# Performance work log

Hardware: AMD Instinct MI355X
Metric: run time of the kernel (lower is better)

## Reference

```python
import jax, jax.numpy as jnp
import numpy as np

H = 1024
N_HEADS = 8
HEAD_DIM = H // N_HEADS
META_DIM = 256
VOCAB = 32000
MIN_W, MAX_W = 0.1, 5.0
LN_EPS = 1e-5


def _ln(x, g, b):
    mu = jnp.mean(x, axis=-1, keepdims=True)
    var = jnp.var(x, axis=-1, keepdims=True)
    return (x - mu) * jax.lax.rsqrt(var + LN_EPS) * g + b


def setup_inputs() -> dict:
    key = jax.random.key(0)
    ks = jax.random.split(key, 16)
    B, S = 4, 2048
    s = 0.02
    return {
        "hidden_states": jax.random.normal(ks[0], (B, S, H), jnp.float32),
        "token_ids": jax.random.randint(ks[1], (B, S), 0, VOCAB, jnp.int32),
        "attention_mask": jnp.ones((B, S), jnp.bool_),
        "pos_embed": jax.random.normal(ks[2], (1, S, H), jnp.float32),
        # torch nn.MultiheadAttention params
        "in_proj_w": jax.random.normal(ks[3], (3 * H, H), jnp.float32) * s,
        "in_proj_b": jnp.zeros((3 * H,), jnp.float32),
        "out_w": jax.random.normal(ks[4], (H, H), jnp.float32) * s,
        "out_b": jnp.zeros((H,), jnp.float32),
        # meta_network params (torch Linear convention: y = x @ W.T + b)
        "w1": jax.random.normal(ks[5], (META_DIM, 2 * H), jnp.float32) * s,
        "b1": jnp.zeros((META_DIM,), jnp.float32),
        "g1": jnp.ones((META_DIM,), jnp.float32),
        "beta1": jnp.zeros((META_DIM,), jnp.float32),
        "w2": jax.random.normal(ks[6], (META_DIM // 2, META_DIM), jnp.float32) * s,
        "b2": jnp.zeros((META_DIM // 2,), jnp.float32),
        "g2": jnp.ones((META_DIM // 2,), jnp.float32),
        "beta2": jnp.zeros((META_DIM // 2,), jnp.float32),
        "w3": jax.random.normal(ks[7], (1, META_DIM // 2), jnp.float32) * s,
        "b3": jnp.zeros((1,), jnp.float32),
        # tensorized ImportanceMemory.get_importance: one scalar per vocab id
        "importance_table": jax.random.uniform(ks[8], (VOCAB,), jnp.float32) * 0.1,
    }


def reference(hidden_states, token_ids, attention_mask, pos_embed,
              in_proj_w, in_proj_b, out_w, out_b,
              w1, b1, g1, beta1, w2, b2, g2, beta2, w3, b3,
              importance_table):
    B, S, _ = hidden_states.shape
    x = hidden_states + pos_embed[:, :S, :]

    # MultiheadAttention (batch_first, eval mode -> no dropout)
    qkv = x @ in_proj_w.T + in_proj_b                      # [B,S,3H]
    q, k, v = jnp.split(qkv, 3, axis=-1)
    q = q.reshape(B, S, N_HEADS, HEAD_DIM)
    k = k.reshape(B, S, N_HEADS, HEAD_DIM)
    v = v.reshape(B, S, N_HEADS, HEAD_DIM)
    scores = jnp.einsum('bqhd,bkhd->bhqk', q, k) / jnp.sqrt(jnp.float32(HEAD_DIM))
    scores = jnp.where(attention_mask[:, None, None, :], scores, jnp.float32(-1e9))
    attn = jax.nn.softmax(scores, axis=-1)
    ctx = jnp.einsum('bhqk,bkhd->bqhd', attn, v).reshape(B, S, H)
    attended = ctx @ out_w.T + out_b

    combined = jnp.concatenate([x, attended], axis=-1)     # [B,S,2H]
    h = jax.nn.relu(_ln(combined @ w1.T + b1, g1, beta1))
    h = jax.nn.relu(_ln(h @ w2.T + b2, g2, beta2))
    base_weights = (h @ w3.T + b3).squeeze(-1)             # [B,S]

    # tensorized per-token importance lookup + clamp (manual_weights empty)
    importance = importance_table[token_ids]               # gather [B,S]
    weight = jnp.clip(base_weights * (1.0 + importance), MIN_W, MAX_W)
    return jnp.where(attention_mask, weight, 0.0)
```

## Files before the change

### kernel.cpp

```cpp
#include <hip/hip_runtime.h>
#include <hip/hip_bf16.h>
#include <math.h>

typedef __bf16 bf16;
typedef bf16 bf16x8 __attribute__((ext_vector_type(8)));
typedef bf16 bf16x4 __attribute__((ext_vector_type(4)));
typedef float f32x4 __attribute__((ext_vector_type(4)));

#define HDIM 1024
#define NHEADS 8
#define HD 128
#define MD1 256
#define MD2 128
#define LNEPS 1e-5f

__device__ __forceinline__ f32x4 mfma16(bf16x8 a, bf16x8 b, f32x4 c) {
  return __builtin_amdgcn_mfma_f32_16x16x32_bf16(a, b, c, 0, 0, 0);
}

__device__ __forceinline__ void gload_lds16(const bf16* g, bf16* l) {
  __builtin_amdgcn_global_load_lds(
      (const __attribute__((address_space(1))) void*)g,
      (__attribute__((address_space(3))) void*)l, 16, 0, 0);
}

__global__ __launch_bounds__(256) void k_prep_all(
    const float* __restrict__ hs, const float* __restrict__ pos,
    bf16* __restrict__ xbf, int SH, int nprep,
    const float* __restrict__ inwf, bf16* __restrict__ winp, int n0,
    const float* __restrict__ w1f, bf16* __restrict__ w1b, int n2,
    const float* __restrict__ w2f, bf16* __restrict__ w2b, int n3,
    const float* __restrict__ owf, const float* __restrict__ obf,
    const float* __restrict__ b1f, bf16* __restrict__ Wp,
    float* __restrict__ b1p, int blocks_el) {
  const int bid = blockIdx.x;
  const int tid = threadIdx.x;
  if (bid < blocks_el) {
    int i = (bid * 256 + tid) * 4;
    if (i < nprep) {
      float4 a = *(const float4*)(hs + i);
      float4 p = *(const float4*)(pos + (i % SH));
      bf16x4 o;
      o[0] = (bf16)(a.x + p.x); o[1] = (bf16)(a.y + p.y);
      o[2] = (bf16)(a.z + p.z); o[3] = (bf16)(a.w + p.w);
      *(bf16x4*)(xbf + i) = o;
      return;
    }
    int j = i - nprep;
    const float* s; bf16* d;
    if (j < n0)           { s = inwf + j; d = winp + j; }
    else if (j < n0 + n2) { s = w1f + (j - n0); d = w1b + (j - n0); }
    else                  { s = w2f + (j - n0 - n2); d = w2b + (j - n0 - n2); }
    float4 v = *(const float4*)s;
    bf16x4 o;
    o[0] = (bf16)v.x; o[1] = (bf16)v.y; o[2] = (bf16)v.z; o[3] = (bf16)v.w;
    *(bf16x4*)d = o;
    return;
  }
  if (bid < blocks_el + 64) {
    __shared__ bf16 Bst[64][42];
    const int bid2 = bid - blocks_el;
    const int d0 = (bid2 & 15) * 64, n0w = (bid2 >> 4) * 64;
    const int w = tid >> 6, lane = tid & 63;
    const int quad = lane >> 4, l16 = lane & 15;
    const float* arow = w1f + (size_t)(n0w + w * 16 + l16) * 2048 + 1024;
    f32x4 acc[4] = {};
    for (int k0 = 0; k0 < 1024; k0 += 32) {
      const int kk = tid >> 3, dd8 = (tid & 7) * 8;
      float4 va = *(const float4*)(owf + (size_t)(k0 + kk) * 1024 + d0 + dd8);
      float4 vb = *(const float4*)(owf + (size_t)(k0 + kk) * 1024 + d0 + dd8 + 4);
      __syncthreads();
      Bst[dd8 + 0][kk] = (bf16)va.x; Bst[dd8 + 1][kk] = (bf16)va.y;
      Bst[dd8 + 2][kk] = (bf16)va.z; Bst[dd8 + 3][kk] = (bf16)va.w;
      Bst[dd8 + 4][kk] = (bf16)vb.x; Bst[dd8 + 5][kk] = (bf16)vb.y;
      Bst[dd8 + 6][kk] = (bf16)vb.z; Bst[dd8 + 7][kk] = (bf16)vb.w;
      __syncthreads();
      float4 fa = *(const float4*)(arow + k0 + quad * 8);
      float4 fb = *(const float4*)(arow + k0 + quad * 8 + 4);
      bf16x8 af;
      af[0] = (bf16)fa.x; af[1] = (bf16)fa.y; af[2] = (bf16)fa.z; af[3] = (bf16)fa.w;
      af[4] = (bf16)fb.x; af[5] = (bf16)fb.y; af[6] = (bf16)fb.z; af[7] = (bf16)fb.w;
#pragma unroll
      for (int dg = 0; dg < 4; ++dg) {
        bf16x8 bfr = *(const bf16x8*)&Bst[dg * 16 + l16][quad * 8];
        acc[dg] = mfma16(af, bfr, acc[dg]);
      }
    }
#pragma unroll
    for (int dg = 0; dg < 4; ++dg) {
      const int d = d0 + dg * 16 + l16;
#pragma unroll
      for (int i = 0; i < 4; ++i)
        Wp[(size_t)(n0w + w * 16 + quad * 4 + i) * 1024 + d] = (bf16)acc[dg][i];
    }
    return;
  }
  const int bid3 = bid - blocks_el - 64;
  const int n = bid3 * 64 + (tid >> 2);
  const int jq = tid & 3;
  const float* row = w1f + (size_t)n * 2048 + 1024 + jq * 256;
  const float* obp = obf + jq * 256;
  float acc = 0.f;
  for (int j = 0; j < 256; j += 4) {
    float4 a = *(const float4*)(row + j);
    float4 o = *(const float4*)(obp + j);
    acc += a.x * o.x + a.y * o.y + a.z * o.z + a.w * o.w;
  }
  acc += __shfl_xor(acc, 1);
  acc += __shfl_xor(acc, 2);
  if (jq == 0) b1p[n] = b1f[n] + acc;
}

__global__ __launch_bounds__(256) void k_gemm_qkv(
    const bf16* __restrict__ A, const bf16* __restrict__ Bw,
    const float* __restrict__ bias, bf16* __restrict__ Qo,
    bf16* __restrict__ Ko, bf16* __restrict__ VTo, int S, int K) {
  __shared__ bf16 As[128 * 64];
  __shared__ bf16 Bs[128 * 64];
  const int tid = threadIdx.x;
  const int w = tid >> 6, lane = tid & 63;
  const int quad = lane >> 4, l16 = lane & 15;
  const int wm = w & 1, wn = w >> 1;
  const int tm = blockIdx.x * 128, tn = blockIdx.y * 128;

  const int tq = tid >> 3, t8 = tid & 7;
  const bf16 *ap[4], *bp[4];
#pragma unroll
  for (int c = 0; c < 4; ++c) {
    const int r = c * 32 + tq;
    const int col = ((t8 ^ ((r ^ (r >> 3)) & 7)) * 8);
    ap[c] = A + (size_t)(tm + r) * K + col;
    bp[c] = Bw + (size_t)(tn + r) * K + col;
  }
  bf16* lA = As + (size_t)tid * 8;
  bf16* lB = Bs + (size_t)tid * 8;

  int fam[4], fbn[4], ram[4], rbn[4];
#pragma unroll
  for (int mt = 0; mt < 4; ++mt) {
    const int r = wm * 64 + mt * 16 + l16;
    ram[mt] = r; fam[mt] = (r ^ (r >> 3)) & 7;
    const int r2 = wn * 64 + mt * 16 + l16;
    rbn[mt] = r2; fbn[mt] = (r2 ^ (r2 >> 3)) & 7;
  }

  f32x4 acc[4][4] = {};
  for (int k0 = 0; k0 < K; k0 += 64) {
#pragma unroll
    for (int c = 0; c < 4; ++c) {
      gload_lds16(ap[c] + k0, lA + c * 2048);
      gload_lds16(bp[c] + k0, lB + c * 2048);
    }
    __syncthreads();
#pragma unroll
    for (int ks = 0; ks < 2; ++ks) {
      bf16x8 af[4], bfr[4];
#pragma unroll
      for (int mt = 0; mt < 4; ++mt)
        af[mt] = *(const bf16x8*)&As[ram[mt] * 64 + (((ks * 4 + quad) ^ fam[mt]) << 3)];
#pragma unroll
      for (int nt = 0; nt < 4; ++nt)
        bfr[nt] = *(const bf16x8*)&Bs[rbn[nt] * 64 + (((ks * 4 + quad) ^ fbn[nt]) << 3)];
#pragma unroll
      for (int mt = 0; mt < 4; ++mt)
#pragma unroll
        for (int nt = 0; nt < 4; ++nt)
          acc[mt][nt] = mfma16(af[mt], bfr[nt], acc[mt][nt]);
    }
    __syncthreads();
  }

  const int region = tn >> 10;
  const int btile = tm / S, s0 = tm % S;
#pragma unroll
  for (int nt = 0; nt < 4; ++nt) {
    const int col = tn + wn * 64 + nt * 16 + l16;
    const float bv = bias[col];
#pragma unroll
    for (int mt = 0; mt < 4; ++mt) {
      if (region == 2) {
        const int d = col - 2048, hh = d >> 7, dd = d & 127;
        const int sb = s0 + wm * 64 + mt * 16 + quad * 4;
        bf16x4 o4;
#pragma unroll
        for (int i = 0; i < 4; ++i) o4[i] = (bf16)(acc[mt][nt][i] + bv);
        *(bf16x4*)&VTo[((size_t)(btile * NHEADS + hh) * HD + dd) * S + sb] = o4;
      } else {
        bf16* dst = (region == 0) ? Qo : Ko;
        const int cc = (region == 0) ? col : col - 1024;
#pragma unroll
        for (int i = 0; i < 4; ++i) {
          const int row = tm + wm * 64 + mt * 16 + quad * 4 + i;
          dst[(size_t)row * HDIM + cc] = (bf16)(acc[mt][nt][i] + bv);
        }
      }
    }
  }
}

__global__ __launch_bounds__(256) void k_flash(
    const bf16* __restrict__ Qg, const bf16* __restrict__ Kg,
    const bf16* __restrict__ VTg, const int* __restrict__ mask,
    bf16* __restrict__ ctx, int S) {
  __shared__ bf16 Ks[64 * 128];
  __shared__ bf16 Vt[128 * 64];
  __shared__ bf16 Ps[8 * 1024];
  __shared__ float biass[64];
  const int tid = threadIdx.x, w = tid >> 6, lane = tid & 63;
  const int quad = lane >> 4, l16 = lane & 15;
  const int p = blockIdx.x;
  const int bh = (p & 7) * 4 + ((p >> 3) >> 4);
  const int qb = (p >> 3) & 15;
  const int b = bh / NHEADS, h = bh % NHEADS;
  const int q0 = qb * 128 + w * 32;
  const size_t bS = (size_t)b * S;
  const bf16* Qb = Qg + bS * HDIM + h * HD;
  const bf16* Kb = Kg + bS * HDIM + h * HD;
  const bf16* Vb = VTg + (size_t)bh * HD * S;
  const int* mrow = mask + bS;

  const bf16 *ksrc[4], *vsrc[4];
#pragma unroll
  for (int it = 0; it < 4; ++it) {
    const int key = it * 16 + (tid >> 4);
    const int g = tid & 15;
    const int fk = (key ^ (key >> 3)) & 7;
    const int db = (g & 8) | ((g ^ fk) & 7);
    ksrc[it] = Kb + (size_t)key * HDIM + db * 8;
    const int d = it * 32 + (tid >> 3);
    const int kb = (tid & 7) ^ (d & 7);
    vsrc[it] = Vb + (size_t)d * S + kb * 8;
  }

  bf16x8 qf[2][4];
#pragma unroll
  for (int qt = 0; qt < 2; ++qt)
#pragma unroll
    for (int s = 0; s < 4; ++s)
      qf[qt][s] = *(const bf16x8*)(Qb + (size_t)(q0 + qt * 16 + l16) * HDIM + s * 32 + quad * 8);

  float lsum[2] = {0.f, 0.f};
  f32x4 o[2][8] = {};
  const float scale2 = 0.08838834764831845f * 1.4426950408889634f;
  const int nchunk = S / 64;

  for (int c0 = 0; c0 < nchunk; ++c0) {
    __syncthreads();
#pragma unroll
    for (int it = 0; it < 4; ++it) {
      gload_lds16(ksrc[it], Ks + it * 2048 + tid * 8);
      gload_lds16(vsrc[it], Vt + it * 2048 + tid * 8);
      ksrc[it] += 64 * HDIM;
      vsrc[it] += 64;
    }
    if (tid < 64) biass[tid] = mrow[c0 * 64 + tid] ? 0.f : -1e9f;
    __syncthreads();

    f32x4 s4[2][4] = {};
#pragma unroll
    for (int g = 0; g < 4; ++g) {
      const int key = g * 16 + l16;
      const int fk = (key ^ (key >> 3)) & 7;
#pragma unroll
      for (int s = 0; s < 4; ++s) {
        const int db = s * 4 + quad;
        const int gr = (db & 8) | ((db ^ fk) & 7);
        bf16x8 kf = *(const bf16x8*)&Ks[key * 128 + gr * 8];
        s4[0][g] = mfma16(kf, qf[0][s], s4[0][g]);
        s4[1][g] = mfma16(kf, qf[1][s], s4[1][g]);
      }
    }
#pragma unroll
    for (int qt = 0; qt < 2; ++qt) {
      const int base = (w * 2 + qt) * 1024;
#pragma unroll
      for (int g = 0; g < 4; ++g) {
        bf16x4 pk;
#pragma unroll
        for (int i = 0; i < 4; ++i) {
          const float pv = exp2f(fmaf(s4[qt][g][i], scale2, biass[g * 16 + quad * 4 + i]));
          lsum[qt] += pv;
          pk[i] = (bf16)pv;
        }
        const int sw = (2 * g + (quad >> 1)) ^ (l16 & 7);
        *(bf16x4*)&Ps[base + l16 * 64 + sw * 8 + (quad & 1) * 4] = pk;
      }
    }
#pragma unroll
    for (int kk = 0; kk < 2; ++kk) {
      const int kb = kk * 4 + quad;
      bf16x8 pf0 = *(const bf16x8*)&Ps[(w * 2) * 1024 + l16 * 64 + ((kb ^ (l16 & 7)) << 3)];
      bf16x8 pf1 = *(const bf16x8*)&Ps[(w * 2 + 1) * 1024 + l16 * 64 + ((kb ^ (l16 & 7)) << 3)];
#pragma unroll
      for (int dg = 0; dg < 8; ++dg) {
        const int d = dg * 16 + l16;
        bf16x8 vf = *(const bf16x8*)&Vt[d * 64 + ((kb ^ (d & 7)) << 3)];
        o[0][dg] = mfma16(pf0, vf, o[0][dg]);
        o[1][dg] = mfma16(pf1, vf, o[1][dg]);
      }
    }
  }

#pragma unroll
  for (int qt = 0; qt < 2; ++qt) {
    lsum[qt] += __shfl_xor(lsum[qt], 16);
    lsum[qt] += __shfl_xor(lsum[qt], 32);
  }
#pragma unroll
  for (int qt = 0; qt < 2; ++qt)
#pragma unroll
    for (int i = 0; i < 4; ++i) {
      const float ls = __shfl(lsum[qt], quad * 4 + i);
      const float inv = 1.0f / ls;
      const int row = q0 + qt * 16 + quad * 4 + i;
#pragma unroll
      for (int dg = 0; dg < 8; ++dg)
        ctx[(bS + row) * HDIM + h * HD + dg * 16 + l16] = (bf16)(o[qt][dg][i] * inv);
    }
}

__global__ __launch_bounds__(256) void k_meta12(
    const bf16* __restrict__ A1, const bf16* __restrict__ A2,
    const bf16* __restrict__ Bw1, const bf16* __restrict__ Wp,
    const float* __restrict__ b1p, const float* __restrict__ g1,
    const float* __restrict__ be1,
    const bf16* __restrict__ Bw2, const float* __restrict__ b2,
    const float* __restrict__ g2, const float* __restrict__ be2,
    const float* __restrict__ w3, const float* __restrict__ b3,
    const int* __restrict__ tok, const int* __restrict__ msk,
    const float* __restrict__ imp, float* __restrict__ out) {
  __shared__ char smem[44032];
  __shared__ float part_s[64][4];
  __shared__ float part_q[64][4];
  bf16 (*As)[40]  = (bf16(*)[40])smem;
  bf16 (*Bs)[40]  = (bf16(*)[40])(smem + 5120);
  bf16 (*h1s)[264] = (bf16(*)[264])smem;
  bf16 (*Bs2)[40] = (bf16(*)[40])(smem + 33792);
  const int tid = threadIdx.x;
  const int w = tid >> 6, lane = tid & 63;
  const int quad = lane >> 4, l16 = lane & 15;
  const int tm = blockIdx.x * 64;
  const int lr = tid >> 2, lc = (tid & 3) * 8;

  f32x4 acc[4][4] = {};
  for (int k0 = 0; k0 < 2048; k0 += 32) {
    const int kg = k0 + lc;
    const bf16* ap = (kg < 1024) ? (A1 + (size_t)(tm + lr) * 1024 + kg)
                                 : (A2 + (size_t)(tm + lr) * 1024 + (kg - 1024));
    *(bf16x8*)&As[lr][lc] = *(const bf16x8*)ap;
#pragma unroll
    for (int it = 0; it < 4; ++it) {
      const int row = lr + it * 64;
      const bf16* bp = (kg < 1024) ? (Bw1 + (size_t)row * 2048 + kg)
                                   : (Wp + (size_t)row * 1024 + (kg - 1024));
      *(bf16x8*)&Bs[row][lc] = *(const bf16x8*)bp;
    }
    __syncthreads();
    bf16x8 af[4], bfr[4];
#pragma unroll
    for (int mt = 0; mt < 4; ++mt) af[mt] = *(const bf16x8*)&As[mt * 16 + l16][quad * 8];
#pragma unroll
    for (int nt = 0; nt < 4; ++nt)
      bfr[nt] = *(const bf16x8*)&Bs[w * 64 + nt * 16 + l16][quad * 8];
#pragma unroll
    for (int mt = 0; mt < 4; ++mt)
#pragma unroll
      for (int nt = 0; nt < 4; ++nt)
        acc[mt][nt] = mfma16(af[mt], bfr[nt], acc[mt][nt]);
    __syncthreads();
  }

  float bv[4], gv[4], bev[4];
#pragma unroll
  for (int nt = 0; nt < 4; ++nt) {
    const int col = w * 64 + nt * 16 + l16;
    bv[nt] = b1p[col]; gv[nt] = g1[col]; bev[nt] = be1[col];
  }
#pragma unroll
  for (int mt = 0; mt < 4; ++mt)
#pragma unroll
    for (int i = 0; i < 4; ++i) {
      float s = 0.f, q = 0.f;
#pragma unroll
      for (int nt = 0; nt < 4; ++nt) {
        const float v = acc[mt][nt][i] + bv[nt];
        s += v; q += v * v;
      }
#pragma unroll
      for (int off = 1; off < 16; off <<= 1) { s += __shfl_xor(s, off); q += __shfl_xor(q, off); }
      if (l16 == 0) {
        const int row = mt * 16 + quad * 4 + i;
        part_s[row][w] = s; part_q[row][w] = q;
      }
    }
  __syncthreads();
#pragma unroll
  for (int mt = 0; mt < 4; ++mt)
#pragma unroll
    for (int i = 0; i < 4; ++i) {
      const int row = mt * 16 + quad * 4 + i;
      const float4 ps = *(const float4*)part_s[row];
      const float4 pq = *(const float4*)part_q[row];
      const float sum = ps.x + ps.y + ps.z + ps.w;
      const float sq = pq.x + pq.y + pq.z + pq.w;
      const float mean = sum / MD1;
      const float var = sq / MD1 - mean * mean;
      const float r = rsqrtf(var + LNEPS);
#pragma unroll
      for (int nt = 0; nt < 4; ++nt) {
        const int col = w * 64 + nt * 16 + l16;
        const float v = acc[mt][nt][i] + bv[nt];
        const float t = (v - mean) * r * gv[nt] + bev[nt];
        h1s[row][col] = (bf16)fmaxf(t, 0.f);
      }
    }
  __syncthreads();

  f32x4 acc2[8] = {};
  for (int k0 = 0; k0 < MD1; k0 += 32) {
    const int kg = k0 + lc;
#pragma unroll
    for (int it = 0; it < 2; ++it)
      *(bf16x8*)&Bs2[lr + it * 64][lc] =
          *(const bf16x8*)(Bw2 + (size_t)(lr + it * 64) * MD1 + kg);
    __syncthreads();
    bf16x8 af = *(const bf16x8*)&h1s[w * 16 + l16][k0 + quad * 8];
#pragma unroll
    for (int nt = 0; nt < 8; ++nt) {
      bf16x8 bfr = *(const bf16x8*)&Bs2[nt * 16 + l16][quad * 8];
      acc2[nt] = mfma16(af, bfr, acc2[nt]);
    }
    __syncthreads();
  }

  float bv2[8], gv2[8], bev2[8], w3v[8];
#pragma unroll
  for (int nt = 0; nt < 8; ++nt) {
    const int col = nt * 16 + l16;
    bv2[nt] = b2[col]; gv2[nt] = g2[col]; bev2[nt] = be2[col]; w3v[nt] = w3[col];
  }
  const float b3v = b3[0];
#pragma unroll
  for (int i = 0; i < 4; ++i) {
    float s = 0.f, q = 0.f;
#pragma unroll
    for (int nt = 0; nt < 8; ++nt) {
      const float v = acc2[nt][i] + bv2[nt];
      s += v; q += v * v;
    }
#pragma unroll
    for (int off = 1; off < 16; off <<= 1) { s += __shfl_xor(s, off); q += __shfl_xor(q, off); }
    const float mean = s / MD2;
    const float var = q / MD2 - mean * mean;
    const float r = rsqrtf(var + LNEPS);
    float d = 0.f;
#pragma unroll
    for (int nt = 0; nt < 8; ++nt) {
      const float v = acc2[nt][i] + bv2[nt];
      const float t = (v - mean) * r * gv2[nt] + bev2[nt];
      d += fmaxf(t, 0.f) * w3v[nt];
    }
#pragma unroll
    for (int off = 1; off < 16; off <<= 1) d += __shfl_xor(d, off);
    if (l16 == 0) {
      const int row = tm + w * 16 + quad * 4 + i;
      float wt = (d + b3v) * (1.f + imp[tok[row]]);
      wt = fminf(fmaxf(wt, 0.1f), 5.0f);
      out[row] = msk[row] ? wt : 0.f;
    }
  }
}

extern "C" void kernel_launch(void* const* d_in, const int* in_sizes, int n_in,
                              void* d_out, int out_size, void* d_ws, size_t ws_size,
                              hipStream_t stream) {
  const float* hs  = (const float*)d_in[0];
  const int*   tok = (const int*)d_in[1];
  const int*   msk = (const int*)d_in[2];
  const float* pos = (const float*)d_in[3];
  const float* inw = (const float*)d_in[4];
  const float* inb = (const float*)d_in[5];
  const float* ow  = (const float*)d_in[6];
  const float* ob  = (const float*)d_in[7];
  const float* w1  = (const float*)d_in[8];
  const float* b1  = (const float*)d_in[9];
  const float* g1  = (const float*)d_in[10];
  const float* be1 = (const float*)d_in[11];
  const float* w2  = (const float*)d_in[12];
  const float* b2  = (const float*)d_in[13];
  const float* g2  = (const float*)d_in[14];
  const float* be2 = (const float*)d_in[15];
  const float* w3  = (const float*)d_in[16];
  const float* b3  = (const float*)d_in[17];
  const float* imp = (const float*)d_in[18];

  const int SH = in_sizes[3];
  const int S  = SH / HDIM;
  const int Bsz = in_sizes[0] / SH;
  const int M = Bsz * S;

  char* ws = (char*)d_ws;
  const size_t MB2 = (size_t)M * HDIM * 2;
  size_t off = 0;
  bf16* xbf = (bf16*)(ws + off);  off += MB2;
  bf16* Qb  = (bf16*)(ws + off);  off += MB2;
  bf16* Kb  = (bf16*)(ws + off);  off += MB2;
  bf16* VTb = (bf16*)(ws + off);  off += MB2;
  bf16* ctx = (bf16*)(ws + off);  off += MB2;
  bf16* winp = (bf16*)(ws + off); off += (size_t)3 * HDIM * HDIM * 2;
  bf16* w1b = (bf16*)(ws + off);  off += (size_t)MD1 * 2 * HDIM * 2;
  bf16* w2b = (bf16*)(ws + off);  off += (size_t)MD2 * MD1 * 2;
  bf16* Wp  = (bf16*)(ws + off);  off += (size_t)MD1 * HDIM * 2;
  float* b1p = (float*)(ws + off); off += (size_t)MD1 * 4;

  const int nprep = M * HDIM;
  const int n0 = 3 * HDIM * HDIM, n2 = MD1 * 2 * HDIM, n3 = MD2 * MD1;
  const int blocks_el = (nprep + n0 + n2 + n3) / 4 / 256;
  k_prep_all<<<blocks_el + 64 + MD1 / 64, 256, 0, stream>>>(
      hs, pos, xbf, SH, nprep, inw, winp, n0, w1, w1b, n2, w2, w2b, n3,
      ow, ob, b1, Wp, b1p, blocks_el);
  k_gemm_qkv<<<dim3(M / 128, (3 * HDIM) / 128), 256, 0, stream>>>(
      xbf, winp, inb, Qb, Kb, VTb, S, HDIM);
  k_flash<<<(S / 128) * Bsz * NHEADS, 256, 0, stream>>>(Qb, Kb, VTb, msk, ctx, S);
  k_meta12<<<M / 64, 256, 0, stream>>>(xbf, ctx, w1b, Wp, b1p, g1, be1,
                                       w2b, b2, g2, be2, w3, b3, tok, msk, imp,
                                       (float*)d_out);
}
```

Baseline: 372.3 us.

## Double-buffer K/V tiles in flash attention and keep mask bias in registers

The flash attention loop now prefetches the next K and V chunk into a second LDS buffer while computing on the current one, so each iteration needs one barrier instead of two. Mask values are loaded directly into registers one chunk ahead, which removes the shared bias array and its LDS round trip. This doubles K/V LDS usage to about 80KB per block, which may lower the number of resident blocks per CU.

```diff
diff --git a/kernel.cpp b/kernel.cpp
--- a/kernel.cpp
+++ b/kernel.cpp
@@ -202,10 +202,9 @@
     const bf16* __restrict__ Qg, const bf16* __restrict__ Kg,
     const bf16* __restrict__ VTg, const int* __restrict__ mask,
     bf16* __restrict__ ctx, int S) {
-  __shared__ bf16 Ks[64 * 128];
-  __shared__ bf16 Vt[128 * 64];
+  __shared__ bf16 Ks[2 * 64 * 128];
+  __shared__ bf16 Vt[2 * 128 * 64];
   __shared__ bf16 Ps[8 * 1024];
-  __shared__ float biass[64];
   const int tid = threadIdx.x, w = tid >> 6, lane = tid & 63;
   const int quad = lane >> 4, l16 = lane & 15;
   const int p = blockIdx.x;
@@ -244,17 +243,29 @@
   const float scale2 = 0.08838834764831845f * 1.4426950408889634f;
   const int nchunk = S / 64;
 
+  int4 mcur[4], mnext[4];
+#pragma unroll
+  for (int it = 0; it < 4; ++it) {
+    gload_lds16(ksrc[it], Ks + it * 2048 + tid * 8);  ksrc[it] += 64 * HDIM;
+    gload_lds16(vsrc[it], Vt + it * 2048 + tid * 8);  vsrc[it] += 64;
+  }
+#pragma unroll
+  for (int g = 0; g < 4; ++g) mcur[g] = *(const int4*)&mrow[g * 16 + quad * 4];
+
   for (int c0 = 0; c0 < nchunk; ++c0) {
     __syncthreads();
-#pragma unroll
-    for (int it = 0; it < 4; ++it) {
-      gload_lds16(ksrc[it], Ks + it * 2048 + tid * 8);
-      gload_lds16(vsrc[it], Vt + it * 2048 + tid * 8);
-      ksrc[it] += 64 * HDIM;
-      vsrc[it] += 64;
-    }
-    if (tid < 64) biass[tid] = mrow[c0 * 64 + tid] ? 0.f : -1e9f;
-    __syncthreads();
+    if (c0 + 1 < nchunk) {
+      const int nb = ((c0 + 1) & 1) * 8192;
+#pragma unroll
+      for (int it = 0; it < 4; ++it) {
+        gload_lds16(ksrc[it], Ks + nb + it * 2048 + tid * 8);  ksrc[it] += 64 * HDIM;
+        gload_lds16(vsrc[it], Vt + nb + it * 2048 + tid * 8);  vsrc[it] += 64;
+      }
+#pragma unroll
+      for (int g = 0; g < 4; ++g)
+        mnext[g] = *(const int4*)&mrow[(c0 + 1) * 64 + g * 16 + quad * 4];
+    }
+    const int cb = (c0 & 1) * 8192;
 
     f32x4 s4[2][4] = {};
 #pragma unroll
@@ -265,7 +276,7 @@
       for (int s = 0; s < 4; ++s) {
         const int db = s * 4 + quad;
         const int gr = (db & 8) | ((db ^ fk) & 7);
-        bf16x8 kf = *(const bf16x8*)&Ks[key * 128 + gr * 8];
+        bf16x8 kf = *(const bf16x8*)&Ks[cb + key * 128 + gr * 8];
         s4[0][g] = mfma16(kf, qf[0][s], s4[0][g]);
         s4[1][g] = mfma16(kf, qf[1][s], s4[1][g]);
       }
@@ -278,7 +289,8 @@
         bf16x4 pk;
 #pragma unroll
         for (int i = 0; i < 4; ++i) {
-          const float pv = exp2f(fmaf(s4[qt][g][i], scale2, biass[g * 16 + quad * 4 + i]));
+          const float bias = ((const int*)&mcur[g])[i] ? 0.f : -1e9f;
+          const float pv = exp2f(fmaf(s4[qt][g][i], scale2, bias));
           lsum[qt] += pv;
           pk[i] = (bf16)pv;
         }
@@ -294,11 +306,13 @@
 #pragma unroll
       for (int dg = 0; dg < 8; ++dg) {
         const int d = dg * 16 + l16;
-        bf16x8 vf = *(const bf16x8*)&Vt[d * 64 + ((kb ^ (d & 7)) << 3)];
+        bf16x8 vf = *(const bf16x8*)&Vt[cb + d * 64 + ((kb ^ (d & 7)) << 3)];
         o[0][dg] = mfma16(pf0, vf, o[0][dg]);
         o[1][dg] = mfma16(pf1, vf, o[1][dg]);
       }
     }
+#pragma unroll
+    for (int g = 0; g < 4; ++g) mcur[g] = mnext[g];
   }
 
 #pragma unroll
```

Result: slower. 410.7 us (+10.3%).
